# Optimization experiments

Measured on AMD Instinct MI355X. Metric: run time of the kernel, lower is better.

Reference implementation:

```python
import jax, jax.numpy as jnp
import numpy as np

K, MU, SIGMA = 8, 0.0, 0.1
M, N, D_DIM, T = 512, 1024, 512, 4096


def setup_inputs() -> dict:
    key = jax.random.key(0)
    ks, ke, ka, kd, kl1, kl2 = jax.random.split(key, 6)
    S = jax.random.normal(ks, (N, T), dtype=jnp.float32)
    E = jax.random.normal(ke, (M, T), dtype=jnp.float32)  # raw noise; scaled by sigma/mu in reference
    A = jax.random.uniform(ka, (M, N), dtype=jnp.float32)  # torch.rand init
    Dm = jax.random.normal(kd, (N, D_DIM), dtype=jnp.float32) / jnp.sqrt(N)  # stands in for DCT-transformed randn
    c = jnp.ones((1,), dtype=jnp.float32)
    l1 = 0.1 * jnp.abs(jax.random.normal(kl1, (1,), dtype=jnp.float32)) + 0.05
    l2 = jax.random.normal(kl2, (1,), dtype=jnp.float32)
    # LISTA params per layer; all K layers get the same closed-form init in the original
    U1 = jnp.eye(D_DIM, dtype=jnp.float32) - (1.0 / c[0]) * (Dm.T @ A.T @ A @ Dm)  # [d,d]
    V1 = (1.0 / c[0]) * (Dm.T @ A.T)  # [d,m]
    U = jnp.broadcast_to(U1, (K, D_DIM, D_DIM)).copy()
    V = jnp.broadcast_to(V1, (K, D_DIM, M)).copy()
    H0 = jnp.zeros((D_DIM, T), dtype=jnp.float32)
    return {"S": S, "E": E, "A": A, "D": Dm, "U": U, "V": V, "l1": l1, "l2": l2, "c": c, "H0": H0}


def reference(S, E, A, D, U, V, l1, l2, c, H0):
    # X = A @ S + noise (E ~ randn, scaled as in torch forward)
    X = A @ S + (E * SIGMA + MU)  # [m,T]
    # Self-attention on H0 (the original loop always feeds self.H, the zero buffer,
    # into every layer -- H is never chained). Attention map = softmax((D@H0)^T (D@H0)).
    G = D @ H0                                   # [n,T]
    attn = jax.nn.softmax(G.T @ G, axis=-1)      # [T,T]
    Z = l2[0] * (H0 @ attn)                      # [d,T]
    # All K LISTA updates share the same (H0-derived) Z and X -> batch over layers.
    mat = jnp.einsum('kde,et->kdt', U, Z) + jnp.einsum('kdm,mt->kdt', V, X)  # [K,d,T]
    thres = l1[0] / c[0]
    H_all = jnp.sign(mat) * jnp.maximum(jnp.zeros((), mat.dtype), jnp.abs(mat) - thres)
    H_last = H_all[-1]                           # only the last layer's H survives the loop
    return D @ H_last                            # S_star [n,T]
```

## Files before the change

### kernel.cpp

```cpp
#include <hip/hip_runtime.h>

typedef unsigned short ushort_t;
typedef unsigned int u32;
typedef ushort_t u16x8 __attribute__((ext_vector_type(8)));
typedef ushort_t u16x4 __attribute__((ext_vector_type(4)));
typedef __bf16   bf16x8 __attribute__((ext_vector_type(8)));
typedef float    f32x4  __attribute__((ext_vector_type(4)));

#define T_DIM 4096

__device__ __forceinline__ ushort_t f2bf(float f){
  union { float f; unsigned u; } x; x.f = f;
  unsigned r = x.u + 0x7FFFu + ((x.u >> 16) & 1u);
  return (ushort_t)(r >> 16);
}

__device__ __forceinline__ void gload16(const void* g, void* l){
  __builtin_amdgcn_global_load_lds(
      (const __attribute__((address_space(1))) u32*)g,
      (__attribute__((address_space(3))) u32*)l, 16, 0, 0);
}

__global__ __launch_bounds__(256) void prep_kernel(
    const float* __restrict__ S, const float* __restrict__ A,
    const float* __restrict__ V7, const float* __restrict__ Dm,
    ushort_t* __restrict__ St, ushort_t* __restrict__ Abf,
    ushort_t* __restrict__ Vbf, ushort_t* __restrict__ Dbf)
{
  __shared__ float tile[64][65];
  const int bid = blockIdx.x, tid = threadIdx.x;
  if (bid < 1024){
    const int t0 = (bid & 63) * 64, n0 = (bid >> 6) * 64;
#pragma unroll
    for (int i = 0; i < 4; ++i){
      int g = tid + 256 * i; int row = g >> 4, cq = g & 15;
      const f32x4 v = *(const f32x4*)&S[(size_t)(n0 + row) * T_DIM + t0 + cq * 4];
#pragma unroll
      for (int j = 0; j < 4; ++j) tile[row][cq * 4 + j] = v[j];
    }
    __syncthreads();
#pragma unroll
    for (int i = 0; i < 2; ++i){
      int g = tid + 256 * i; int tl = g >> 3, nq = g & 7;
      u16x8 h;
#pragma unroll
      for (int j = 0; j < 8; ++j) h[j] = f2bf(tile[nq * 8 + j][tl]);
      *(u16x8*)&St[(size_t)(t0 + tl) * 1024 + n0 + ((nq ^ (tl & 7)) << 3)] = h;
    }
  } else {
    int pid = bid - 1024;
    const float* src; ushort_t* dst; int g, ks;
    if (pid < 256)      { src = A;  dst = Abf; g = pid * 256 + tid;        ks = 7; }
    else if (pid < 384) { src = V7; dst = Vbf; g = (pid - 256) * 256 + tid; ks = 6; }
    else                { src = Dm; dst = Dbf; g = (pid - 384) * 256 + tid; ks = 6; }
    const int r = g >> ks, cg = g & ((1 << ks) - 1);
    const int Kd = 8 << ks;
    const size_t base = (size_t)r * Kd + (size_t)cg * 8;
    const f32x4 v0 = *(const f32x4*)&src[base];
    const f32x4 v1 = *(const f32x4*)&src[base + 4];
    u16x8 h;
#pragma unroll
    for (int j = 0; j < 4; ++j){ h[j] = f2bf(v0[j]); h[j + 4] = f2bf(v1[j]); }
    *(u16x8*)&dst[(size_t)r * Kd + ((cg >> 3) << 6) + ((((cg & 7) ^ (r & 7))) << 3)] = h;
  }
}

template<int EPI, int KD>
__global__ __launch_bounds__(512) void gemm_kernel(
    const ushort_t* __restrict__ Ag, const ushort_t* __restrict__ Bg,
    void* __restrict__ Cout, const float* __restrict__ Eptr,
    const float* __restrict__ l1p, const float* __restrict__ cp)
{
  constexpr int NK = KD / 64;
  constexpr bool SWAP = (EPI != 2);
  __shared__ __align__(16) ushort_t As[3][128 * 64];
  __shared__ __align__(16) ushort_t Bs[3][64 * 64];
  const int tid = threadIdx.x;
  const int lane = tid & 63, wid = tid >> 6;
  const int wm = wid >> 1, wn = wid & 1;
  const int lr = lane & 15, lq = lane >> 4;
  const int t0 = blockIdx.x * 128, n0 = blockIdx.y * 64;

  f32x4 acc[2][2];
#pragma unroll
  for (int i = 0; i < 2; ++i)
#pragma unroll
    for (int j = 0; j < 2; ++j) acc[i][j] = (f32x4){0.f, 0.f, 0.f, 0.f};

  auto stage = [&](int kt, int b){
#pragma unroll
    for (int i = 0; i < 2; ++i){
      int c = i * 512 + tid;
      gload16(&Ag[(size_t)(t0 + (c >> 3)) * KD + kt * 64 + (c & 7) * 8],
              &As[b][(i * 512 + (tid & 448)) * 8]);
    }
    {
      int c = tid;
      gload16(&Bg[(size_t)(n0 + (c >> 3)) * KD + kt * 64 + (c & 7) * 8],
              &Bs[b][(tid & 448) * 8]);
    }
  };

  auto compute = [&](int b){
#pragma unroll
    for (int ksv = 0; ksv < 2; ++ksv){
      const int kb = ksv * 4 + lq;
      bf16x8 a[2], bb[2];
#pragma unroll
      for (int mf = 0; mf < 2; ++mf){
        int r = wm * 32 + mf * 16 + lr;
        a[mf] = *(const bf16x8*)&As[b][r * 64 + ((kb ^ (r & 7)) << 3)];
      }
#pragma unroll
      for (int nf = 0; nf < 2; ++nf){
        int r = wn * 32 + nf * 16 + lr;
        bb[nf] = *(const bf16x8*)&Bs[b][r * 64 + ((kb ^ (r & 7)) << 3)];
      }
      __builtin_amdgcn_s_setprio(1);
      if constexpr (SWAP){
#pragma unroll
        for (int nf = 0; nf < 2; ++nf)
#pragma unroll
          for (int mf = 0; mf < 2; ++mf)
            acc[nf][mf] = __builtin_amdgcn_mfma_f32_16x16x32_bf16(
                bb[nf], a[mf], acc[nf][mf], 0, 0, 0);
      } else {
#pragma unroll
        for (int mf = 0; mf < 2; ++mf)
#pragma unroll
          for (int nf = 0; nf < 2; ++nf)
            acc[mf][nf] = __builtin_amdgcn_mfma_f32_16x16x32_bf16(
                a[mf], bb[nf], acc[mf][nf], 0, 0, 0);
      }
      __builtin_amdgcn_s_setprio(0);
    }
  };

  stage(0, 0);
  stage(1, 1);
  for (int kt = 0; kt < NK; ++kt){
    if (kt < NK - 1) { asm volatile("s_waitcnt vmcnt(3)" ::: "memory"); }
    else             { asm volatile("s_waitcnt vmcnt(0)" ::: "memory"); }
    __builtin_amdgcn_s_barrier();
    __builtin_amdgcn_sched_barrier(0);
    if (kt + 2 < NK) stage(kt + 2, (kt + 2) % 3);
    compute(kt % 3);
  }

  if constexpr (EPI == 2){
    float* O = (float*)Cout;
#pragma unroll
    for (int mf = 0; mf < 2; ++mf)
#pragma unroll
      for (int nf = 0; nf < 2; ++nf){
        const int t = t0 + wm * 32 + mf * 16 + lq * 4;
        const int n = n0 + wn * 32 + nf * 16 + lr;
        *(f32x4*)&O[(size_t)n * T_DIM + t] = acc[mf][nf];
      }
  } else {
    const float thres = (EPI == 1) ? (l1p[0] / cp[0]) : 0.f;
    ushort_t* OT = (ushort_t*)Cout;
#pragma unroll
    for (int nf = 0; nf < 2; ++nf){
#pragma unroll
      for (int mf = 0; mf < 2; ++mf){
        const int m = n0 + wn * 32 + nf * 16 + lq * 4;
        const int t = t0 + wm * 32 + mf * 16 + lr;
        f32x4 v = acc[nf][mf];
        u16x4 h;
        if constexpr (EPI == 0){
#pragma unroll
          for (int j = 0; j < 4; ++j){
            float e = Eptr[(size_t)(m + j) * T_DIM + t];
            h[j] = f2bf(v[j] + 0.1f * e);
          }
        } else {
#pragma unroll
          for (int j = 0; j < 4; ++j){
            float av = fabsf(v[j]) - thres;
            float r = av > 0.f ? (v[j] > 0.f ? av : -av) : 0.f;
            h[j] = f2bf(r);
          }
        }
        *(u16x4*)&OT[(size_t)t * 512 + (m & ~63) +
                     (((((m >> 3) & 7) ^ (t & 7))) << 3) + (m & 7)] = h;
      }
    }
  }
}

extern "C" void kernel_launch(void* const* d_in, const int* in_sizes, int n_in,
                              void* d_out, int out_size, void* d_ws, size_t ws_size,
                              hipStream_t stream)
{
  const float* S  = (const float*)d_in[0];
  const float* E  = (const float*)d_in[1];
  const float* A  = (const float*)d_in[2];
  const float* Dm = (const float*)d_in[3];
  const float* V  = (const float*)d_in[5];
  const float* l1 = (const float*)d_in[6];
  const float* c  = (const float*)d_in[8];

  char* ws = (char*)d_ws;
  ushort_t* St  = (ushort_t*)(ws);
  ushort_t* XT  = (ushort_t*)(ws + (size_t)( 8u << 20));
  ushort_t* HT  = (ushort_t*)(ws + (size_t)(12u << 20));
  ushort_t* Abf = (ushort_t*)(ws + (size_t)(16u << 20));
  ushort_t* Vbf = (ushort_t*)(ws + (size_t)(17u << 20));
  ushort_t* Dbf = (ushort_t*)(ws + (size_t)(17u << 20) + (512u << 10));
  const float* V7 = V + (size_t)7 * 512 * 512;

  prep_kernel<<<1664, 256, 0, stream>>>(S, A, V7, Dm, St, Abf, Vbf, Dbf);
  gemm_kernel<0, 1024><<<dim3(32, 8), 512, 0, stream>>>(St, Abf, (void*)XT, E, nullptr, nullptr);
  gemm_kernel<1, 512><<<dim3(32, 8), 512, 0, stream>>>(XT, Vbf, (void*)HT, nullptr, l1, c);
  gemm_kernel<2, 512><<<dim3(32, 16), 512, 0, stream>>>(HT, Dbf, d_out, nullptr, nullptr, nullptr);
}
```

Measured before the change: 40.02 us.

## Split-K the first two GEMMs and fuse partial reduction into consumer A-loads

```diff
diff --git a/kernel.cpp b/kernel.cpp
--- a/kernel.cpp
+++ b/kernel.cpp
@@ -65,14 +65,12 @@
   }
 }
 
-template<int EPI, int KD>
-__global__ __launch_bounds__(512) void gemm_kernel(
+__global__ __launch_bounds__(512, 4) void gemm1_kernel(
     const ushort_t* __restrict__ Ag, const ushort_t* __restrict__ Bg,
-    void* __restrict__ Cout, const float* __restrict__ Eptr,
-    const float* __restrict__ l1p, const float* __restrict__ cp)
+    float* __restrict__ Xp0, float* __restrict__ Xp1,
+    const float* __restrict__ Eptr)
 {
-  constexpr int NK = KD / 64;
-  constexpr bool SWAP = (EPI != 2);
+  constexpr int NK = 8;
   __shared__ __align__(16) ushort_t As[3][128 * 64];
   __shared__ __align__(16) ushort_t Bs[3][64 * 64];
   const int tid = threadIdx.x;
@@ -80,6 +78,7 @@
   const int wm = wid >> 1, wn = wid & 1;
   const int lr = lane & 15, lq = lane >> 4;
   const int t0 = blockIdx.x * 128, n0 = blockIdx.y * 64;
+  const int koff = blockIdx.z * 512;
 
   f32x4 acc[2][2];
 #pragma unroll
@@ -91,14 +90,11 @@
 #pragma unroll
     for (int i = 0; i < 2; ++i){
       int c = i * 512 + tid;
-      gload16(&Ag[(size_t)(t0 + (c >> 3)) * KD + kt * 64 + (c & 7) * 8],
+      gload16(&Ag[(size_t)(t0 + (c >> 3)) * 1024 + koff + kt * 64 + (c & 7) * 8],
               &As[b][(i * 512 + (tid & 448)) * 8]);
     }
-    {
-      int c = tid;
-      gload16(&Bg[(size_t)(n0 + (c >> 3)) * KD + kt * 64 + (c & 7) * 8],
-              &Bs[b][(tid & 448) * 8]);
-    }
+    gload16(&Bg[(size_t)(n0 + (tid >> 3)) * 1024 + koff + kt * 64 + (tid & 7) * 8],
+            &Bs[b][(tid & 448) * 8]);
   };
 
   auto compute = [&](int b){
@@ -117,21 +113,12 @@
         bb[nf] = *(const bf16x8*)&Bs[b][r * 64 + ((kb ^ (r & 7)) << 3)];
       }
       __builtin_amdgcn_s_setprio(1);
-      if constexpr (SWAP){
-#pragma unroll
-        for (int nf = 0; nf < 2; ++nf)
-#pragma unroll
-          for (int mf = 0; mf < 2; ++mf)
-            acc[nf][mf] = __builtin_amdgcn_mfma_f32_16x16x32_bf16(
-                bb[nf], a[mf], acc[nf][mf], 0, 0, 0);
-      } else {
+#pragma unroll
+      for (int nf = 0; nf < 2; ++nf)
 #pragma unroll
         for (int mf = 0; mf < 2; ++mf)
-#pragma unroll
-          for (int nf = 0; nf < 2; ++nf)
-            acc[mf][nf] = __builtin_amdgcn_mfma_f32_16x16x32_bf16(
-                a[mf], bb[nf], acc[mf][nf], 0, 0, 0);
-      }
+          acc[nf][mf] = __builtin_amdgcn_mfma_f32_16x16x32_bf16(
+              bb[nf], a[mf], acc[nf][mf], 0, 0, 0);
       __builtin_amdgcn_s_setprio(0);
     }
   };
@@ -147,8 +134,142 @@
     compute(kt % 3);
   }
 
-  if constexpr (EPI == 2){
-    float* O = (float*)Cout;
+  float* Out = blockIdx.z == 0 ? Xp0 : Xp1;
+#pragma unroll
+  for (int nf = 0; nf < 2; ++nf){
+#pragma unroll
+    for (int mf = 0; mf < 2; ++mf){
+      const int m = n0 + wn * 32 + nf * 16 + lq * 4;
+      const int t = t0 + wm * 32 + mf * 16 + lr;
+      f32x4 v = acc[nf][mf];
+      if (blockIdx.z == 0){
+#pragma unroll
+        for (int j = 0; j < 4; ++j)
+          v[j] += 0.1f * Eptr[(size_t)(m + j) * T_DIM + t];
+      }
+      *(f32x4*)&Out[(size_t)t * 512 + m] = v;
+    }
+  }
+}
+
+template<int FINAL, int NK>
+__global__ __launch_bounds__(512, 4) void gemm_regA_kernel(
+    const float* __restrict__ Ap0, const float* __restrict__ Ap1,
+    const ushort_t* __restrict__ Bg, float* __restrict__ Out0,
+    float* __restrict__ Out1, const float* __restrict__ l1p,
+    const float* __restrict__ cp)
+{
+  __shared__ __align__(16) ushort_t As[2][128 * 64];
+  __shared__ __align__(16) ushort_t Bs[3][64 * 64];
+  const int tid = threadIdx.x;
+  const int lane = tid & 63, wid = tid >> 6;
+  const int wm = wid >> 1, wn = wid & 1;
+  const int lr = lane & 15, lq = lane >> 4;
+  const int t0 = blockIdx.x * 128, n0 = blockIdx.y * 64;
+  const int koff = FINAL ? 0 : blockIdx.z * 256;
+  const float thres = FINAL ? (l1p[0] / cp[0]) : 0.f;
+
+  f32x4 acc[2][2];
+#pragma unroll
+  for (int i = 0; i < 2; ++i)
+#pragma unroll
+    for (int j = 0; j < 2; ++j) acc[i][j] = (f32x4){0.f, 0.f, 0.f, 0.f};
+
+  f32x4 rA[8];
+
+  auto loadA = [&](int kt){
+#pragma unroll
+    for (int i = 0; i < 2; ++i){
+      int c = i * 512 + tid;
+      const size_t ix = (size_t)(t0 + (c >> 3)) * 512 + koff + kt * 64 + (c & 7) * 8;
+      rA[i * 4 + 0] = *(const f32x4*)&Ap0[ix];
+      rA[i * 4 + 1] = *(const f32x4*)&Ap0[ix + 4];
+      rA[i * 4 + 2] = *(const f32x4*)&Ap1[ix];
+      rA[i * 4 + 3] = *(const f32x4*)&Ap1[ix + 4];
+    }
+  };
+
+  auto dsWriteA = [&](int b){
+#pragma unroll
+    for (int i = 0; i < 2; ++i){
+      int c = i * 512 + tid;
+      const int row = c >> 3, kb = c & 7;
+      u16x8 h;
+#pragma unroll
+      for (int j = 0; j < 4; ++j){
+        float s0 = rA[i * 4 + 0][j] + rA[i * 4 + 2][j];
+        float s1 = rA[i * 4 + 1][j] + rA[i * 4 + 3][j];
+        if (FINAL){
+          float a0 = fabsf(s0) - thres;
+          s0 = a0 > 0.f ? (s0 > 0.f ? a0 : -a0) : 0.f;
+          float a1 = fabsf(s1) - thres;
+          s1 = a1 > 0.f ? (s1 > 0.f ? a1 : -a1) : 0.f;
+        }
+        h[j] = f2bf(s0); h[j + 4] = f2bf(s1);
+      }
+      *(u16x8*)&As[b][row * 64 + ((kb ^ (row & 7)) << 3)] = h;
+    }
+  };
+
+  auto stageB = [&](int kt, int b){
+    gload16(&Bg[(size_t)(n0 + (tid >> 3)) * 512 + koff + kt * 64 + (tid & 7) * 8],
+            &Bs[b][(tid & 448) * 8]);
+  };
+
+  auto compute = [&](int ab, int bb_){
+#pragma unroll
+    for (int ksv = 0; ksv < 2; ++ksv){
+      const int kb = ksv * 4 + lq;
+      bf16x8 a[2], bb[2];
+#pragma unroll
+      for (int mf = 0; mf < 2; ++mf){
+        int r = wm * 32 + mf * 16 + lr;
+        a[mf] = *(const bf16x8*)&As[ab][r * 64 + ((kb ^ (r & 7)) << 3)];
+      }
+#pragma unroll
+      for (int nf = 0; nf < 2; ++nf){
+        int r = wn * 32 + nf * 16 + lr;
+        bb[nf] = *(const bf16x8*)&Bs[bb_][r * 64 + ((kb ^ (r & 7)) << 3)];
+      }
+      __builtin_amdgcn_s_setprio(1);
+      if constexpr (!FINAL){
+#pragma unroll
+        for (int nf = 0; nf < 2; ++nf)
+#pragma unroll
+          for (int mf = 0; mf < 2; ++mf)
+            acc[nf][mf] = __builtin_amdgcn_mfma_f32_16x16x32_bf16(
+                bb[nf], a[mf], acc[nf][mf], 0, 0, 0);
+      } else {
+#pragma unroll
+        for (int mf = 0; mf < 2; ++mf)
+#pragma unroll
+          for (int nf = 0; nf < 2; ++nf)
+            acc[mf][nf] = __builtin_amdgcn_mfma_f32_16x16x32_bf16(
+                a[mf], bb[nf], acc[mf][nf], 0, 0, 0);
+      }
+      __builtin_amdgcn_s_setprio(0);
+    }
+  };
+
+  loadA(0);
+  asm volatile("s_waitcnt vmcnt(0)" ::: "memory");
+  dsWriteA(0);
+  loadA(1);
+  stageB(0, 0); stageB(1, 1);
+
+  for (int kt = 0; kt < NK; ++kt){
+    if (kt < NK - 1) { asm volatile("s_waitcnt vmcnt(1)" ::: "memory"); }
+    else             { asm volatile("s_waitcnt vmcnt(0)" ::: "memory"); }
+    asm volatile("s_waitcnt lgkmcnt(0)" ::: "memory");
+    __builtin_amdgcn_s_barrier();
+    __builtin_amdgcn_sched_barrier(0);
+    if (kt + 1 < NK) dsWriteA((kt + 1) & 1);
+    if (kt + 2 < NK) { loadA(kt + 2); stageB(kt + 2, (kt + 2) % 3); }
+    compute(kt & 1, kt % 3);
+  }
+
+  if constexpr (FINAL){
+    float* O = Out0;
 #pragma unroll
     for (int mf = 0; mf < 2; ++mf)
 #pragma unroll
@@ -158,34 +279,15 @@
         *(f32x4*)&O[(size_t)n * T_DIM + t] = acc[mf][nf];
       }
   } else {
-    const float thres = (EPI == 1) ? (l1p[0] / cp[0]) : 0.f;
-    ushort_t* OT = (ushort_t*)Cout;
-#pragma unroll
-    for (int nf = 0; nf < 2; ++nf){
+    float* O = blockIdx.z == 0 ? Out0 : Out1;
+#pragma unroll
+    for (int nf = 0; nf < 2; ++nf)
 #pragma unroll
       for (int mf = 0; mf < 2; ++mf){
         const int m = n0 + wn * 32 + nf * 16 + lq * 4;
         const int t = t0 + wm * 32 + mf * 16 + lr;
-        f32x4 v = acc[nf][mf];
-        u16x4 h;
-        if constexpr (EPI == 0){
-#pragma unroll
-          for (int j = 0; j < 4; ++j){
-            float e = Eptr[(size_t)(m + j) * T_DIM + t];
-            h[j] = f2bf(v[j] + 0.1f * e);
-          }
-        } else {
-#pragma unroll
-          for (int j = 0; j < 4; ++j){
-            float av = fabsf(v[j]) - thres;
-            float r = av > 0.f ? (v[j] > 0.f ? av : -av) : 0.f;
-            h[j] = f2bf(r);
-          }
-        }
-        *(u16x4*)&OT[(size_t)t * 512 + (m & ~63) +
-                     (((((m >> 3) & 7) ^ (t & 7))) << 3) + (m & 7)] = h;
-      }
-    }
+        *(f32x4*)&O[(size_t)t * 512 + m] = acc[nf][mf];
+      }
   }
 }
 
@@ -203,15 +305,19 @@
 
   char* ws = (char*)d_ws;
   ushort_t* St  = (ushort_t*)(ws);
-  ushort_t* XT  = (ushort_t*)(ws + (size_t)( 8u << 20));
-  ushort_t* HT  = (ushort_t*)(ws + (size_t)(12u << 20));
-  ushort_t* Abf = (ushort_t*)(ws + (size_t)(16u << 20));
-  ushort_t* Vbf = (ushort_t*)(ws + (size_t)(17u << 20));
-  ushort_t* Dbf = (ushort_t*)(ws + (size_t)(17u << 20) + (512u << 10));
+  ushort_t* Abf = (ushort_t*)(ws + (size_t)( 8u << 20));
+  ushort_t* Vbf = (ushort_t*)(ws + (size_t)( 9u << 20));
+  ushort_t* Dbf = (ushort_t*)(ws + (size_t)(10u << 20));
+  float*    Xp0 = (float*)   (ws + (size_t)(16u << 20));
+  float*    Xp1 = (float*)   (ws + (size_t)(24u << 20));
+  float*    Hp0 = (float*)   (ws + (size_t)(32u << 20));
+  float*    Hp1 = (float*)   (ws + (size_t)(40u << 20));
   const float* V7 = V + (size_t)7 * 512 * 512;
 
   prep_kernel<<<1664, 256, 0, stream>>>(S, A, V7, Dm, St, Abf, Vbf, Dbf);
-  gemm_kernel<0, 1024><<<dim3(32, 8), 512, 0, stream>>>(St, Abf, (void*)XT, E, nullptr, nullptr);
-  gemm_kernel<1, 512><<<dim3(32, 8), 512, 0, stream>>>(XT, Vbf, (void*)HT, nullptr, l1, c);
-  gemm_kernel<2, 512><<<dim3(32, 16), 512, 0, stream>>>(HT, Dbf, d_out, nullptr, nullptr, nullptr);
-}
+  gemm1_kernel<<<dim3(32, 8, 2), 512, 0, stream>>>(St, Abf, Xp0, Xp1, E);
+  gemm_regA_kernel<0, 4><<<dim3(32, 8, 2), 512, 0, stream>>>(
+      Xp0, Xp1, Vbf, Hp0, Hp1, nullptr, nullptr);
+  gemm_regA_kernel<1, 8><<<dim3(32, 16, 1), 512, 0, stream>>>(
+      Hp0, Hp1, Dbf, (float*)d_out, nullptr, l1, c);
+}
```

New measurement: 54.47 us. 36.1% more time.

## Fuse prep and three GEMMs into one persistent kernel with grid barriers

Applied to the files above, without the earlier changes.

```diff
diff --git a/kernel.cpp b/kernel.cpp
--- a/kernel.cpp
+++ b/kernel.cpp
@@ -3,7 +3,6 @@
 typedef unsigned short ushort_t;
 typedef unsigned int u32;
 typedef ushort_t u16x8 __attribute__((ext_vector_type(8)));
-typedef ushort_t u16x4 __attribute__((ext_vector_type(4)));
 typedef __bf16   bf16x8 __attribute__((ext_vector_type(8)));
 typedef float    f32x4  __attribute__((ext_vector_type(4)));
 
@@ -21,65 +20,30 @@
       (__attribute__((address_space(3))) u32*)l, 16, 0, 0);
 }
 
-__global__ __launch_bounds__(256) void prep_kernel(
-    const float* __restrict__ S, const float* __restrict__ A,
-    const float* __restrict__ V7, const float* __restrict__ Dm,
-    ushort_t* __restrict__ St, ushort_t* __restrict__ Abf,
-    ushort_t* __restrict__ Vbf, ushort_t* __restrict__ Dbf)
+__device__ __forceinline__ void gbar(unsigned* bar, unsigned target){
+  __syncthreads();
+  if (threadIdx.x == 0){
+    __threadfence();
+    atomicAdd(bar, 1u);
+    while (atomicAdd(bar, 0u) < target) __builtin_amdgcn_s_sleep(8);
+    __threadfence();
+  }
+  __syncthreads();
+}
+
+template<int EPI, int NK>
+__device__ void gemm_body(
+    ushort_t* __restrict__ AsB, ushort_t* __restrict__ BsB,
+    const ushort_t* __restrict__ Ag, const ushort_t* __restrict__ Bg,
+    void* __restrict__ Cout, const float* __restrict__ Eptr, float thres,
+    int t0, int n0)
 {
-  __shared__ float tile[64][65];
-  const int bid = blockIdx.x, tid = threadIdx.x;
-  if (bid < 1024){
-    const int t0 = (bid & 63) * 64, n0 = (bid >> 6) * 64;
-#pragma unroll
-    for (int i = 0; i < 4; ++i){
-      int g = tid + 256 * i; int row = g >> 4, cq = g & 15;
-      const f32x4 v = *(const f32x4*)&S[(size_t)(n0 + row) * T_DIM + t0 + cq * 4];
-#pragma unroll
-      for (int j = 0; j < 4; ++j) tile[row][cq * 4 + j] = v[j];
-    }
-    __syncthreads();
-#pragma unroll
-    for (int i = 0; i < 2; ++i){
-      int g = tid + 256 * i; int tl = g >> 3, nq = g & 7;
-      u16x8 h;
-#pragma unroll
-      for (int j = 0; j < 8; ++j) h[j] = f2bf(tile[nq * 8 + j][tl]);
-      *(u16x8*)&St[(size_t)(t0 + tl) * 1024 + n0 + ((nq ^ (tl & 7)) << 3)] = h;
-    }
-  } else {
-    int pid = bid - 1024;
-    const float* src; ushort_t* dst; int g, ks;
-    if (pid < 256)      { src = A;  dst = Abf; g = pid * 256 + tid;        ks = 7; }
-    else if (pid < 384) { src = V7; dst = Vbf; g = (pid - 256) * 256 + tid; ks = 6; }
-    else                { src = Dm; dst = Dbf; g = (pid - 384) * 256 + tid; ks = 6; }
-    const int r = g >> ks, cg = g & ((1 << ks) - 1);
-    const int Kd = 8 << ks;
-    const size_t base = (size_t)r * Kd + (size_t)cg * 8;
-    const f32x4 v0 = *(const f32x4*)&src[base];
-    const f32x4 v1 = *(const f32x4*)&src[base + 4];
-    u16x8 h;
-#pragma unroll
-    for (int j = 0; j < 4; ++j){ h[j] = f2bf(v0[j]); h[j + 4] = f2bf(v1[j]); }
-    *(u16x8*)&dst[(size_t)r * Kd + ((cg >> 3) << 6) + ((((cg & 7) ^ (r & 7))) << 3)] = h;
-  }
-}
-
-template<int EPI, int KD>
-__global__ __launch_bounds__(512) void gemm_kernel(
-    const ushort_t* __restrict__ Ag, const ushort_t* __restrict__ Bg,
-    void* __restrict__ Cout, const float* __restrict__ Eptr,
-    const float* __restrict__ l1p, const float* __restrict__ cp)
-{
-  constexpr int NK = KD / 64;
+  constexpr int KD = NK * 64;
   constexpr bool SWAP = (EPI != 2);
-  __shared__ __align__(16) ushort_t As[3][128 * 64];
-  __shared__ __align__(16) ushort_t Bs[3][64 * 64];
   const int tid = threadIdx.x;
   const int lane = tid & 63, wid = tid >> 6;
   const int wm = wid >> 1, wn = wid & 1;
   const int lr = lane & 15, lq = lane >> 4;
-  const int t0 = blockIdx.x * 128, n0 = blockIdx.y * 64;
 
   f32x4 acc[2][2];
 #pragma unroll
@@ -88,20 +52,21 @@
     for (int j = 0; j < 2; ++j) acc[i][j] = (f32x4){0.f, 0.f, 0.f, 0.f};
 
   auto stage = [&](int kt, int b){
+    ushort_t* As = AsB + b * 8192;
+    ushort_t* Bs = BsB + b * 4096;
 #pragma unroll
     for (int i = 0; i < 2; ++i){
       int c = i * 512 + tid;
       gload16(&Ag[(size_t)(t0 + (c >> 3)) * KD + kt * 64 + (c & 7) * 8],
-              &As[b][(i * 512 + (tid & 448)) * 8]);
-    }
-    {
-      int c = tid;
-      gload16(&Bg[(size_t)(n0 + (c >> 3)) * KD + kt * 64 + (c & 7) * 8],
-              &Bs[b][(tid & 448) * 8]);
-    }
+              &As[(i * 512 + (tid & 448)) * 8]);
+    }
+    gload16(&Bg[(size_t)(n0 + (tid >> 3)) * KD + kt * 64 + (tid & 7) * 8],
+            &Bs[(tid & 448) * 8]);
   };
 
   auto compute = [&](int b){
+    ushort_t* As = AsB + b * 8192;
+    ushort_t* Bs = BsB + b * 4096;
 #pragma unroll
     for (int ksv = 0; ksv < 2; ++ksv){
       const int kb = ksv * 4 + lq;
@@ -109,12 +74,12 @@
 #pragma unroll
       for (int mf = 0; mf < 2; ++mf){
         int r = wm * 32 + mf * 16 + lr;
-        a[mf] = *(const bf16x8*)&As[b][r * 64 + ((kb ^ (r & 7)) << 3)];
+        a[mf] = *(const bf16x8*)&As[r * 64 + ((kb ^ (r & 7)) << 3)];
       }
 #pragma unroll
       for (int nf = 0; nf < 2; ++nf){
         int r = wn * 32 + nf * 16 + lr;
-        bb[nf] = *(const bf16x8*)&Bs[b][r * 64 + ((kb ^ (r & 7)) << 3)];
+        bb[nf] = *(const bf16x8*)&Bs[r * 64 + ((kb ^ (r & 7)) << 3)];
       }
       __builtin_amdgcn_s_setprio(1);
       if constexpr (SWAP){
@@ -158,7 +123,6 @@
         *(f32x4*)&O[(size_t)n * T_DIM + t] = acc[mf][nf];
       }
   } else {
-    const float thres = (EPI == 1) ? (l1p[0] / cp[0]) : 0.f;
     ushort_t* OT = (ushort_t*)Cout;
 #pragma unroll
     for (int nf = 0; nf < 2; ++nf){
@@ -167,7 +131,7 @@
         const int m = n0 + wn * 32 + nf * 16 + lq * 4;
         const int t = t0 + wm * 32 + mf * 16 + lr;
         f32x4 v = acc[nf][mf];
-        u16x4 h;
+        ushort_t h[4];
         if constexpr (EPI == 0){
 #pragma unroll
           for (int j = 0; j < 4; ++j){
@@ -182,11 +146,88 @@
             h[j] = f2bf(r);
           }
         }
-        *(u16x4*)&OT[(size_t)t * 512 + (m & ~63) +
-                     (((((m >> 3) & 7) ^ (t & 7))) << 3) + (m & 7)] = h;
-      }
-    }
-  }
+        *(__attribute__((ext_vector_type(4))) ushort_t*)
+            &OT[(size_t)t * 512 + (m & ~63) +
+                (((((m >> 3) & 7) ^ (t & 7))) << 3) + (m & 7)] =
+            *(__attribute__((ext_vector_type(4))) ushort_t*)h;
+      }
+    }
+  }
+}
+
+__global__ __launch_bounds__(512, 2) void fused_kernel(
+    const float* __restrict__ S, const float* __restrict__ E,
+    const float* __restrict__ A, const float* __restrict__ Dm,
+    const float* __restrict__ V7, const float* __restrict__ l1p,
+    const float* __restrict__ cp,
+    ushort_t* __restrict__ St, ushort_t* __restrict__ XT,
+    ushort_t* __restrict__ HT, ushort_t* __restrict__ Abf,
+    ushort_t* __restrict__ Vbf, ushort_t* __restrict__ Dbf,
+    float* __restrict__ out, unsigned* __restrict__ bar)
+{
+  __shared__ __align__(16) ushort_t LDSBUF[43008];
+  ushort_t* AsB = LDSBUF;
+  ushort_t* BsB = LDSBUF + 24576;
+  float (*tile)[65] = (float(*)[65])LDSBUF;
+
+  const int tid = threadIdx.x;
+  const int b = blockIdx.x;
+  const int x = b & 31, y = b >> 5;
+
+#pragma unroll 1
+  for (int i = 0; i < 2; ++i){
+#pragma unroll 1
+    for (int j = 0; j < 2; ++j){
+      const int tt0 = (2 * x + i) * 64, nn0 = (2 * y + j) * 64;
+#pragma unroll
+      for (int it = 0; it < 2; ++it){
+        int g = it * 512 + tid; int row = g >> 4, cq = g & 15;
+        const f32x4 v = *(const f32x4*)&S[(size_t)(nn0 + row) * T_DIM + tt0 + cq * 4];
+#pragma unroll
+        for (int jj = 0; jj < 4; ++jj) tile[row][cq * 4 + jj] = v[jj];
+      }
+      __syncthreads();
+      {
+        int tl = tid >> 3, nq = tid & 7;
+        u16x8 h;
+#pragma unroll
+        for (int jj = 0; jj < 8; ++jj) h[jj] = f2bf(tile[nq * 8 + jj][tl]);
+        *(u16x8*)&St[(size_t)(tt0 + tl) * 1024 + nn0 + ((nq ^ (tl & 7)) << 3)] = h;
+      }
+      __syncthreads();
+    }
+  }
+#pragma unroll 1
+  for (int pass = 0; pass < 2; ++pass){
+    const int cidx = b + pass * 256;
+    if (cidx < 320){
+      const float* src; ushort_t* dst; int g, ks;
+      if (cidx < 128)      { src = A;  dst = Abf; g = cidx * 512 + tid;         ks = 7; }
+      else if (cidx < 192) { src = V7; dst = Vbf; g = (cidx - 128) * 512 + tid; ks = 6; }
+      else                 { src = Dm; dst = Dbf; g = (cidx - 192) * 512 + tid; ks = 6; }
+      const int r = g >> ks, cg = g & ((1 << ks) - 1);
+      const int Kd = 8 << ks;
+      const size_t base = (size_t)r * Kd + (size_t)cg * 8;
+      const f32x4 v0 = *(const f32x4*)&src[base];
+      const f32x4 v1 = *(const f32x4*)&src[base + 4];
+      u16x8 h;
+#pragma unroll
+      for (int jj = 0; jj < 4; ++jj){ h[jj] = f2bf(v0[jj]); h[jj + 4] = f2bf(v1[jj]); }
+      *(u16x8*)&dst[(size_t)r * Kd + ((cg >> 3) << 6) + ((((cg & 7) ^ (r & 7))) << 3)] = h;
+    }
+  }
+  gbar(bar, 256);
+
+  gemm_body<0, 16>(AsB, BsB, St, Abf, (void*)XT, E, 0.f, x * 128, y * 64);
+  gbar(bar, 512);
+
+  const float thres = l1p[0] / cp[0];
+  gemm_body<1, 8>(AsB, BsB, XT, Vbf, (void*)HT, nullptr, thres, x * 128, y * 64);
+  gbar(bar, 768);
+
+  gemm_body<2, 8>(AsB, BsB, HT, Dbf, (void*)out, nullptr, 0.f, x * 128, y * 64);
+  __syncthreads();
+  gemm_body<2, 8>(AsB, BsB, HT, Dbf, (void*)out, nullptr, 0.f, x * 128, (y + 8) * 64);
 }
 
 extern "C" void kernel_launch(void* const* d_in, const int* in_sizes, int n_in,
@@ -208,10 +249,11 @@
   ushort_t* Abf = (ushort_t*)(ws + (size_t)(16u << 20));
   ushort_t* Vbf = (ushort_t*)(ws + (size_t)(17u << 20));
   ushort_t* Dbf = (ushort_t*)(ws + (size_t)(17u << 20) + (512u << 10));
+  unsigned* bar = (unsigned*)(ws + (size_t)(19u << 20));
   const float* V7 = V + (size_t)7 * 512 * 512;
 
-  prep_kernel<<<1664, 256, 0, stream>>>(S, A, V7, Dm, St, Abf, Vbf, Dbf);
-  gemm_kernel<0, 1024><<<dim3(32, 8), 512, 0, stream>>>(St, Abf, (void*)XT, E, nullptr, nullptr);
-  gemm_kernel<1, 512><<<dim3(32, 8), 512, 0, stream>>>(XT, Vbf, (void*)HT, nullptr, l1, c);
-  gemm_kernel<2, 512><<<dim3(32, 16), 512, 0, stream>>>(HT, Dbf, d_out, nullptr, nullptr, nullptr);
-}
+  hipMemsetAsync(bar, 0, 4, stream);
+  fused_kernel<<<256, 512, 0, stream>>>(S, E, A, Dm, V7, l1, c,
+                                        St, XT, HT, Abf, Vbf, Dbf,
+                                        (float*)d_out, bar);
+}
```

After: 105.3 us. 2.63x slower.
